# Kernel optimization log

Hardware: AMD Instinct MI355X
Metric: run time of the kernel (lower is better)

The kernel has to match this reference:

```python
import jax, jax.numpy as jnp
import numpy as np

MODEL_DIM = 1024
PROBE_RANK = 128

def setup_inputs() -> dict:
    key = jax.random.key(0)
    k1, k2 = jax.random.split(key)
    batch = jax.random.normal(k1, (8, 512, MODEL_DIM), dtype=jnp.float32)
    # nn.init.uniform_(proj, -0.05, 0.05)
    proj = jax.random.uniform(k2, (MODEL_DIM, PROBE_RANK), dtype=jnp.float32,
                              minval=-0.05, maxval=0.05)
    return {"batch": batch, "proj": proj}

def reference(batch, proj):
    # [B, S, R] low-rank projection
    transformed = jnp.matmul(batch, proj)
    # pairwise squared L2 distances via broadcast: [B, S, 1, R] - [B, 1, S, R]
    diffs = transformed[:, :, None, :] - transformed[:, None, :, :]
    squared_distances = jnp.sum(diffs * diffs, axis=-1)  # [B, S, S]
    return squared_distances
```

## Files before the change

### kernel.cpp

```cpp
#include <hip/hip_runtime.h>
#include <hip/hip_bf16.h>


#define S_DIM 512
#define K_DIM 1024
#define R_DIM 128
#define M_ROWS 4096

typedef __attribute__((ext_vector_type(8))) short short8;
typedef __attribute__((ext_vector_type(4))) float float4v;

__device__ unsigned short g_projB[(K_DIM / 8) * R_DIM * 8];
__device__ unsigned short g_Tf[8 * (R_DIM / 8) * S_DIM * 8];
__device__ float g_norms[M_ROWS];

__device__ __forceinline__ unsigned short f2b(float f) {
  unsigned int u = __builtin_bit_cast(unsigned int, f);
  u += 0x7FFFu + ((u >> 16) & 1u);
  return (unsigned short)(u >> 16);
}
__device__ __forceinline__ float b2f(unsigned short b) {
  unsigned int u = ((unsigned int)b) << 16;
  return __builtin_bit_cast(float, u);
}

__global__ __launch_bounds__(256) void prep_proj(const float* __restrict__ proj) {
  const int t = threadIdx.x;
  const int k = blockIdx.x * 8 + (t >> 5);
  const int n4 = (t & 31) * 4;
  const float4 v = *(const float4*)(proj + (size_t)k * R_DIM + n4);
  const unsigned short b0 = f2b(v.x), b1 = f2b(v.y), b2 = f2b(v.z), b3 = f2b(v.w);
  const int q = k >> 3, j = k & 7;
  g_projB[((size_t)q * R_DIM + n4 + 0) * 8 + j] = b0;
  g_projB[((size_t)q * R_DIM + n4 + 1) * 8 + j] = b1;
  g_projB[((size_t)q * R_DIM + n4 + 2) * 8 + j] = b2;
  g_projB[((size_t)q * R_DIM + n4 + 3) * 8 + j] = b3;
}

__global__ __launch_bounds__(512) void transform_kernel(const float* __restrict__ batch) {
  __shared__ __attribute__((aligned(16))) unsigned short As[2][8 * 16 * 8];
  __shared__ __attribute__((aligned(16))) unsigned short Bs[2][8 * 128 * 8];
  __shared__ float sh_norm[16];

  const int t = threadIdx.x;
  if (t < 16) sh_norm[t] = 0.0f;
  const int M0 = blockIdx.x * 16;
  const int lane = t & 63;
  const int wave = t >> 6;
  const int quad = lane >> 4;
  const int l16 = lane & 15;
  const int n0 = wave * 16;

  const int am = t >> 4;
  const int ai = t & 15;
  const float* aptr = batch + (size_t)(M0 + am) * K_DIM + ai * 4;
  const unsigned short* bptr = g_projB + (size_t)t * 16;

  float4 apv = {0, 0, 0, 0};
  uint4 bpv0, bpv1;
  if (t < 256) apv = *(const float4*)(aptr);
  bpv0 = *(const uint4*)(bptr);
  bpv1 = *(const uint4*)(bptr + 8);

  float4v acc = {0.f, 0.f, 0.f, 0.f};

  for (int c = 0; c < 16; c++) {
    const int buf = c & 1;
    if (t < 256) {
      unsigned short* dst = &As[buf][(((ai >> 1) * 16 + am) * 8) + (ai & 1) * 4];
      uint2 packed;
      packed.x = (unsigned int)f2b(apv.x) | ((unsigned int)f2b(apv.y) << 16);
      packed.y = (unsigned int)f2b(apv.z) | ((unsigned int)f2b(apv.w) << 16);
      *(uint2*)dst = packed;
    }
    *(uint4*)(&Bs[buf][t * 16]) = bpv0;
    *(uint4*)(&Bs[buf][t * 16 + 8]) = bpv1;
    __syncthreads();
    if (c < 15) {
      if (t < 256) apv = *(const float4*)(aptr + (c + 1) * 64);
      bpv0 = *(const uint4*)(bptr + (size_t)(c + 1) * 8192);
      bpv1 = *(const uint4*)(bptr + (size_t)(c + 1) * 8192 + 8);
    }
#pragma unroll
    for (int ks = 0; ks < 2; ks++) {
      const int q64 = ks * 4 + quad;
      const short8 af = *(const short8*)(&As[buf][(q64 * 16 + l16) * 8]);
      const short8 bf = *(const short8*)(&Bs[buf][(q64 * 128 + n0 + l16) * 8]);
      acc = __builtin_amdgcn_mfma_f32_16x16x32_bf16(af, bf, acc, 0, 0, 0);
    }
  }

  const int n = n0 + l16;
  float sq[4];
#pragma unroll
  for (int r = 0; r < 4; r++) {
    const unsigned short tb = f2b(acc[r]);
    const float tv = b2f(tb);
    sq[r] = tv * tv;
    const int gm = M0 + quad * 4 + r;
    const int bidx = gm >> 9, row = gm & 511;
    g_Tf[(((size_t)bidx * 16 + (n >> 3)) * S_DIM + row) * 8 + (n & 7)] = tb;
  }
#pragma unroll
  for (int r = 0; r < 4; r++) {
    float v = sq[r];
    v += __shfl_xor(v, 1);
    v += __shfl_xor(v, 2);
    v += __shfl_xor(v, 4);
    v += __shfl_xor(v, 8);
    if (l16 == 0) atomicAdd(&sh_norm[quad * 4 + r], v);
  }
  __syncthreads();
  if (t < 16) g_norms[M0 + t] = sh_norm[t];
}

__global__ __launch_bounds__(256) void dist_kernel(float* __restrict__ out) {
  const int t = threadIdx.x;
  const int lane = t & 63;
  const int wave = t >> 6;
  const int quad = lane >> 4;
  const int l16 = lane & 15;
  const int b = blockIdx.z;
  const int i0 = blockIdx.y * 64 + wave * 16;
  const int j0 = blockIdx.x * 64;

  const unsigned short* Tb = g_Tf + (size_t)b * 16 * S_DIM * 8;

  short8 af[4];
#pragma unroll
  for (int ks = 0; ks < 4; ks++) {
    const int q64 = ks * 4 + quad;
    af[ks] = *(const short8*)(Tb + ((size_t)q64 * S_DIM + i0 + l16) * 8);
  }
  short8 bfr[4][4];
#pragma unroll
  for (int jt = 0; jt < 4; jt++)
#pragma unroll
    for (int ks = 0; ks < 4; ks++) {
      const int q64 = ks * 4 + quad;
      bfr[jt][ks] = *(const short8*)(Tb + ((size_t)q64 * S_DIM + j0 + jt * 16 + l16) * 8);
    }

  float4v acc[4];
#pragma unroll
  for (int jt = 0; jt < 4; jt++) acc[jt] = (float4v){0.f, 0.f, 0.f, 0.f};
#pragma unroll
  for (int jt = 0; jt < 4; jt++)
#pragma unroll
    for (int ks = 0; ks < 4; ks++)
      acc[jt] = __builtin_amdgcn_mfma_f32_16x16x32_bf16(af[ks], bfr[jt][ks], acc[jt], 0, 0, 0);

  const float* nb = g_norms + (size_t)b * S_DIM;
  float ni[4];
#pragma unroll
  for (int r = 0; r < 4; r++) ni[r] = nb[i0 + quad * 4 + r];

  float* ob = out + (size_t)b * S_DIM * S_DIM;
#pragma unroll
  for (int jt = 0; jt < 4; jt++) {
    const float nj = nb[j0 + jt * 16 + l16];
#pragma unroll
    for (int r = 0; r < 4; r++) {
      const int i = i0 + quad * 4 + r;
      const int j = j0 + jt * 16 + l16;
      ob[(size_t)i * S_DIM + j] = ni[r] + nj - 2.0f * acc[jt][r];
    }
  }
}

extern "C" void kernel_launch(void* const* d_in, const int* in_sizes, int n_in,
                              void* d_out, int out_size, void* d_ws, size_t ws_size,
                              hipStream_t stream) {
  const float* batch = (const float*)d_in[0];
  const float* proj = (const float*)d_in[1];
  float* out = (float*)d_out;
  hipLaunchKernelGGL(prep_proj, dim3(128), dim3(256), 0, stream, proj);
  hipLaunchKernelGGL(transform_kernel, dim3(256), dim3(512), 0, stream, batch);
  hipLaunchKernelGGL(dist_kernel, dim3(8, 8, 8), dim3(256), 0, stream, out);
}
```

Before: 81.15 us.

## Split transform GEMM across N halves with larger K chunks and partial norms

The transform kernel now launches a 2x256 grid of 256-thread blocks, each computing 64 of the 128 projection columns for 16 rows. Each loop iteration stages 128 K elements, so there are 8 iterations instead of 16, with every thread doing the loads. Each block writes a partial row norm to one of two buffers, and the distance kernel adds the two halves. This doubles the number of blocks to use more CUs and cuts barrier count, at the cost of reading every batch row twice and a few extra norm loads.

```diff
diff --git a/kernel.cpp b/kernel.cpp
--- a/kernel.cpp
+++ b/kernel.cpp
@@ -12,7 +12,7 @@
 
 __device__ unsigned short g_projB[(K_DIM / 8) * R_DIM * 8];
 __device__ unsigned short g_Tf[8 * (R_DIM / 8) * S_DIM * 8];
-__device__ float g_norms[M_ROWS];
+__device__ float g_normsP[2][M_ROWS];
 
 __device__ __forceinline__ unsigned short f2b(float f) {
   unsigned int u = __builtin_bit_cast(unsigned int, f);
@@ -37,60 +37,69 @@
   g_projB[((size_t)q * R_DIM + n4 + 3) * 8 + j] = b3;
 }
 
-__global__ __launch_bounds__(512) void transform_kernel(const float* __restrict__ batch) {
-  __shared__ __attribute__((aligned(16))) unsigned short As[2][8 * 16 * 8];
-  __shared__ __attribute__((aligned(16))) unsigned short Bs[2][8 * 128 * 8];
+__global__ __launch_bounds__(256) void transform_kernel(const float* __restrict__ batch) {
+  __shared__ __attribute__((aligned(16))) unsigned short As[2][16 * 16 * 8];
+  __shared__ __attribute__((aligned(16))) unsigned short Bs[2][16 * 64 * 8];
   __shared__ float sh_norm[16];
 
   const int t = threadIdx.x;
   if (t < 16) sh_norm[t] = 0.0f;
-  const int M0 = blockIdx.x * 16;
+  const int half = blockIdx.x;
+  const int M0 = blockIdx.y * 16;
+  const int nb64 = half * 64;
   const int lane = t & 63;
   const int wave = t >> 6;
   const int quad = lane >> 4;
   const int l16 = lane & 15;
   const int n0 = wave * 16;
 
-  const int am = t >> 4;
-  const int ai = t & 15;
-  const float* aptr = batch + (size_t)(M0 + am) * K_DIM + ai * 4;
-  const unsigned short* bptr = g_projB + (size_t)t * 16;
+  const int aq = t >> 4;
+  const int am = t & 15;
+  const float* aptr = batch + (size_t)(M0 + am) * K_DIM + aq * 8;
+  const unsigned short* bptr =
+      g_projB + ((size_t)(wave * 4) * R_DIM + nb64 + (t & 63)) * 8;
 
-  float4 apv = {0, 0, 0, 0};
-  uint4 bpv0, bpv1;
-  if (t < 256) apv = *(const float4*)(aptr);
-  bpv0 = *(const uint4*)(bptr);
-  bpv1 = *(const uint4*)(bptr + 8);
+  float4 a0 = *(const float4*)(aptr);
+  float4 a1 = *(const float4*)(aptr + 4);
+  uint4 bv0 = *(const uint4*)(bptr);
+  uint4 bv1 = *(const uint4*)(bptr + R_DIM * 8);
+  uint4 bv2 = *(const uint4*)(bptr + 2 * R_DIM * 8);
+  uint4 bv3 = *(const uint4*)(bptr + 3 * R_DIM * 8);
 
   float4v acc = {0.f, 0.f, 0.f, 0.f};
 
-  for (int c = 0; c < 16; c++) {
+  for (int c = 0; c < 8; c++) {
     const int buf = c & 1;
-    if (t < 256) {
-      unsigned short* dst = &As[buf][(((ai >> 1) * 16 + am) * 8) + (ai & 1) * 4];
-      uint2 packed;
-      packed.x = (unsigned int)f2b(apv.x) | ((unsigned int)f2b(apv.y) << 16);
-      packed.y = (unsigned int)f2b(apv.z) | ((unsigned int)f2b(apv.w) << 16);
-      *(uint2*)dst = packed;
-    }
-    *(uint4*)(&Bs[buf][t * 16]) = bpv0;
-    *(uint4*)(&Bs[buf][t * 16 + 8]) = bpv1;
+    uint4 ap;
+    ap.x = (unsigned int)f2b(a0.x) | ((unsigned int)f2b(a0.y) << 16);
+    ap.y = (unsigned int)f2b(a0.z) | ((unsigned int)f2b(a0.w) << 16);
+    ap.z = (unsigned int)f2b(a1.x) | ((unsigned int)f2b(a1.y) << 16);
+    ap.w = (unsigned int)f2b(a1.z) | ((unsigned int)f2b(a1.w) << 16);
+    *(uint4*)(&As[buf][(size_t)t * 8]) = ap;
+    *(uint4*)(&Bs[buf][((size_t)(wave * 4 + 0) * 64 + (t & 63)) * 8]) = bv0;
+    *(uint4*)(&Bs[buf][((size_t)(wave * 4 + 1) * 64 + (t & 63)) * 8]) = bv1;
+    *(uint4*)(&Bs[buf][((size_t)(wave * 4 + 2) * 64 + (t & 63)) * 8]) = bv2;
+    *(uint4*)(&Bs[buf][((size_t)(wave * 4 + 3) * 64 + (t & 63)) * 8]) = bv3;
     __syncthreads();
-    if (c < 15) {
-      if (t < 256) apv = *(const float4*)(aptr + (c + 1) * 64);
-      bpv0 = *(const uint4*)(bptr + (size_t)(c + 1) * 8192);
-      bpv1 = *(const uint4*)(bptr + (size_t)(c + 1) * 8192 + 8);
+    if (c < 7) {
+      a0 = *(const float4*)(aptr + (c + 1) * 128);
+      a1 = *(const float4*)(aptr + (c + 1) * 128 + 4);
+      const unsigned short* bp = bptr + (size_t)(c + 1) * 16 * R_DIM * 8;
+      bv0 = *(const uint4*)(bp);
+      bv1 = *(const uint4*)(bp + R_DIM * 8);
+      bv2 = *(const uint4*)(bp + 2 * R_DIM * 8);
+      bv3 = *(const uint4*)(bp + 3 * R_DIM * 8);
     }
 #pragma unroll
-    for (int ks = 0; ks < 2; ks++) {
-      const int q64 = ks * 4 + quad;
-      const short8 af = *(const short8*)(&As[buf][(q64 * 16 + l16) * 8]);
-      const short8 bf = *(const short8*)(&Bs[buf][(q64 * 128 + n0 + l16) * 8]);
+    for (int ks = 0; ks < 4; ks++) {
+      const int q = ks * 4 + quad;
+      const short8 af = *(const short8*)(&As[buf][((size_t)q * 16 + l16) * 8]);
+      const short8 bf = *(const short8*)(&Bs[buf][((size_t)q * 64 + n0 + l16) * 8]);
       acc = __builtin_amdgcn_mfma_f32_16x16x32_bf16(af, bf, acc, 0, 0, 0);
     }
   }
 
-  const int n = n0 + l16;
+  const int n = nb64 + n0 + l16;
   float sq[4];
 #pragma unroll
   for (int r = 0; r < 4; r++) {
@@ -111,7 +120,7 @@
     if (l16 == 0) atomicAdd(&sh_norm[quad * 4 + r], v);
   }
   __syncthreads();
-  if (t < 16) g_norms[M0 + t] = sh_norm[t];
+  if (t < 16) g_normsP[half][M0 + t] = sh_norm[t];
 }
 
 __global__ __launch_bounds__(256) void dist_kernel(float* __restrict__ out) {
@@ -150,19 +159,23 @@
     for (int ks = 0; ks < 4; ks++)
       acc[jt] = __builtin_amdgcn_mfma_f32_16x16x32_bf16(af[ks], bfr[jt][ks], acc[jt], 0, 0, 0);
 
-  const float* nb = g_norms + (size_t)b * S_DIM;
+  const float* np0 = g_normsP[0] + (size_t)b * S_DIM;
+  const float* np1 = g_normsP[1] + (size_t)b * S_DIM;
   float ni[4];
 #pragma unroll
-  for (int r = 0; r < 4; r++) ni[r] = nb[i0 + quad * 4 + r];
+  for (int r = 0; r < 4; r++) {
+    const int i = i0 + quad * 4 + r;
+    ni[r] = np0[i] + np1[i];
+  }
 
   float* ob = out + (size_t)b * S_DIM * S_DIM;
 #pragma unroll
   for (int jt = 0; jt < 4; jt++) {
-    const float nj = nb[j0 + jt * 16 + l16];
+    const int j = j0 + jt * 16 + l16;
+    const float nj = np0[j] + np1[j];
 #pragma unroll
     for (int r = 0; r < 4; r++) {
       const int i = i0 + quad * 4 + r;
-      const int j = j0 + jt * 16 + l16;
       ob[(size_t)i * S_DIM + j] = ni[r] + nj - 2.0f * acc[jt][r];
     }
   }
@@ -175,6 +188,6 @@
   const float* proj = (const float*)d_in[1];
   float* out = (float*)d_out;
   hipLaunchKernelGGL(prep_proj, dim3(128), dim3(256), 0, stream, proj);
-  hipLaunchKernelGGL(transform_kernel, dim3(256), dim3(512), 0, stream, batch);
+  hipLaunchKernelGGL(transform_kernel, dim3(2, 256), dim3(256), 0, stream, batch);
   hipLaunchKernelGGL(dist_kernel, dim3(8, 8, 8), dim3(256), 0, stream, out);
 }
```

Result: faster. 76.47 us, median of 2 (-5.8%).
